# Kernel tuning notes

Measured on AMD Instinct MI355X. Metric: run time of the kernel, lower is better.

The kernel has to match this reference:

```python
import jax, jax.numpy as jnp
import numpy as np

B = 1024
NUM_FEATURES = 800  # 10*10 grid * 8 channels
L1, L2, L3, NUM_CLASSES = 1024, 15, 32, 1
STRIDE = 10  # max(1, (96+2*1-3)//(10-1))
VIS_THRESH = 0.0


def setup_inputs() -> dict:
    key = jax.random.key(0)
    ks = jax.random.split(key, 9)
    images = jax.random.normal(ks[0], (B, 3, 96, 96), dtype=jnp.float32)
    conv_w = jax.random.normal(ks[1], (8, 3, 3, 3), dtype=jnp.float32) * 0.1
    ft_w = jax.random.normal(ks[2], (NUM_FEATURES, L1), dtype=jnp.float32) * 0.1
    ft_b = jnp.zeros((L1,), dtype=jnp.float32)
    w1 = jax.random.normal(ks[3], (L2, L1), dtype=jnp.float32) * (1.0 / np.sqrt(L1))
    b1 = jax.random.normal(ks[4], (L2,), dtype=jnp.float32) * 0.01
    w2 = jax.random.normal(ks[5], (L3, L2), dtype=jnp.float32) * (1.0 / np.sqrt(L2))
    b2 = jax.random.normal(ks[6], (L3,), dtype=jnp.float32) * 0.01
    w3 = jax.random.normal(ks[7], (NUM_CLASSES, L3), dtype=jnp.float32) * (1.0 / np.sqrt(L3))
    b3 = jax.random.normal(ks[8], (NUM_CLASSES,), dtype=jnp.float32) * 0.01
    return {"images": images, "conv_w": conv_w, "ft_w": ft_w, "ft_b": ft_b,
            "w1": w1, "b1": b1, "w2": w2, "b2": b2, "w3": w3, "b3": b3}


def reference(images, conv_w, ft_w, ft_b, w1, b1, w2, b2, w3, b3):
    # Conv2d(3->8, k=3, stride=10, pad=1, no bias): [B,3,96,96] -> [B,8,10,10]
    x = jax.lax.conv_general_dilated(
        images, conv_w, window_strides=(STRIDE, STRIDE),
        padding=((1, 1), (1, 1)),
        dimension_numbers=("NCHW", "OIHW", "NCHW"))
    x = jnp.clip(x, -1.0, 1.0)  # Hardtanh
    # training-mode soft binarization
    binary = jax.nn.sigmoid(10.0 * (x - VIS_THRESH))
    bflat = binary.reshape(binary.shape[0], -1)  # [B, 800]
    # _to_sparse_features keeps only entries > 0.5; FeatureTransformer then does
    # a ragged gather-scale-sum == masked dense matmul with the FT weights.
    vals = jnp.where(bflat > 0.5, bflat, 0.0)
    features = vals @ ft_w + ft_b  # [B, L1]
    l0 = jnp.clip(features, 0.0, 1.0)
    h = L1 // 2
    s0, s1 = l0[:, :h], l0[:, h:]
    l0c = jnp.concatenate([s0 * s1, s0], axis=1) * (127.0 / 128.0)  # [B, L1]
    # SimpleClassifier: Linear->ReLU->Linear->ReLU->Linear
    h1 = jax.nn.relu(l0c @ w1.T + b1)
    h2 = jax.nn.relu(h1 @ w2.T + b2)
    out = h2 @ w3.T + b3  # [B, NUM_CLASSES]
    return out
```

## Files before the change

### kernel.cpp

```cpp
#include <hip/hip_runtime.h>

typedef unsigned short u16;
typedef unsigned int   u32;
typedef __attribute__((ext_vector_type(8))) short short8;
typedef __attribute__((ext_vector_type(4))) float f32x4;

__device__ __forceinline__ u16 f2bf(float f) {
    union { float f; u32 i; } v; v.f = f;
    u32 x = v.i;
    return (u16)((x + 0x7fffu + ((x >> 16) & 1u)) >> 16);
}
__device__ __forceinline__ float bf2f(u16 u) {
    union { u32 i; float f; } v; v.i = ((u32)u) << 16; return v.f;
}

__global__ __launch_bounds__(256) void k0_split(
    const float* __restrict__ ft_w,
    u16* __restrict__ bth, u16* __restrict__ btl)
{
    __shared__ float tile[32][33];
    int k0 = blockIdx.x * 32, n0 = blockIdx.y * 32;
    int tx = threadIdx.x & 31, ty = threadIdx.x >> 5;
    #pragma unroll
    for (int i = 0; i < 4; i++) {
        int k = ty + i * 8;
        tile[k][tx] = ft_w[(k0 + k) * 1024 + n0 + tx];
    }
    __syncthreads();
    #pragma unroll
    for (int i = 0; i < 4; i++) {
        int n = ty + i * 8;
        float wv = tile[tx][n];
        u16 hi = f2bf(wv);
        float lo = wv - bf2f(hi);
        bth[(n0 + n) * 800 + k0 + tx] = hi;
        btl[(n0 + n) * 800 + k0 + tx] = f2bf(lo);
    }
}

__global__ __launch_bounds__(256) void k1_conv(
    const float* __restrict__ images,
    const float* __restrict__ conv_w,
    u16* __restrict__ vh, u16* __restrict__ vl)
{
    __shared__ float img_s[3][29][96];
    __shared__ float w[216];

    int b = blockIdx.x;
    int t = threadIdx.x;
    if (t < 216) w[t] = conv_w[t];

    for (int i = t; i < 3 * 29 * 96; i += 256) {
        int ch  = i / (29 * 96);
        int rem = i - ch * (29 * 96);
        int lr  = rem / 96;
        int x   = rem - lr * 96;
        int ih  = 10 * ((lr + 1) / 3) + (lr + 1) % 3 - 1;
        img_s[ch][lr][x] = images[((b * 3 + ch) * 96 + ih) * 96 + x];
    }
    __syncthreads();

    for (int ridx = t; ridx < 800; ridx += 256) {
        int o  = ridx / 100;
        int p  = ridx - o * 100;
        int oh = p / 10;
        int ow = p - oh * 10;

        float sum = 0.0f;
        #pragma unroll
        for (int ic = 0; ic < 3; ic++) {
            const float* wc = &w[o * 27 + ic * 9];
            #pragma unroll
            for (int kh = 0; kh < 3; kh++) {
                int lr = 3 * oh + kh - 1;
                if (lr < 0) continue;
                #pragma unroll
                for (int kw = 0; kw < 3; kw++) {
                    int iw = ow * 10 + kw - 1;
                    if (iw < 0) continue;
                    sum = fmaf(img_s[ic][lr][iw], wc[kh * 3 + kw], sum);
                }
            }
        }
        float xc = fminf(fmaxf(sum, -1.0f), 1.0f);
        float binary = 1.0f / (1.0f + __expf(-10.0f * xc));
        float v = (binary > 0.5f) ? binary : 0.0f;
        u16 hi = f2bf(v);
        vh[b * 800 + ridx] = hi;
        vl[b * 800 + ridx] = f2bf(v - bf2f(hi));
    }
}

__global__ __launch_bounds__(256) void k2_mfma(
    const u16* __restrict__ Ah, const u16* __restrict__ Al,
    const u16* __restrict__ Bh, const u16* __restrict__ Bl,
    const float* __restrict__ bias,
    float* __restrict__ C)
{
    __shared__ u16 sAh[64 * 40], sAl[64 * 40], sBh[64 * 40], sBl[64 * 40];
    int t = threadIdx.x;
    int m0 = blockIdx.y * 64, n0 = blockIdx.x * 64;
    int w = t >> 6, lane = t & 63;
    int quad = lane >> 4, lo4 = lane & 15;
    int wm = (w >> 1) * 32, wn = (w & 1) * 32;

    int sr = t >> 2;
    int sq = t & 3;
    const u16* gAh = Ah + (m0 + sr) * 800 + sq * 8;
    const u16* gAl = Al + (m0 + sr) * 800 + sq * 8;
    const u16* gBh = Bh + (n0 + sr) * 800 + sq * 8;
    const u16* gBl = Bl + (n0 + sr) * 800 + sq * 8;
    int sdst = sr * 40 + sq * 8;

    f32x4 acc[2][2] = {};

    for (int k0 = 0; k0 < 800; k0 += 32) {
        *(uint4*)&sAh[sdst] = *(const uint4*)(gAh + k0);
        *(uint4*)&sAl[sdst] = *(const uint4*)(gAl + k0);
        *(uint4*)&sBh[sdst] = *(const uint4*)(gBh + k0);
        *(uint4*)&sBl[sdst] = *(const uint4*)(gBl + k0);
        __syncthreads();

        short8 a_h[2], a_l[2], b_h[2], b_l[2];
        #pragma unroll
        for (int f = 0; f < 2; f++) {
            int mi = (wm + f * 16 + lo4) * 40 + quad * 8;
            a_h[f] = *(const short8*)&sAh[mi];
            a_l[f] = *(const short8*)&sAl[mi];
            int ni = (wn + f * 16 + lo4) * 40 + quad * 8;
            b_h[f] = *(const short8*)&sBh[ni];
            b_l[f] = *(const short8*)&sBl[ni];
        }
        #pragma unroll
        for (int fm = 0; fm < 2; fm++)
            #pragma unroll
            for (int fn = 0; fn < 2; fn++) {
                acc[fm][fn] = __builtin_amdgcn_mfma_f32_16x16x32_bf16(a_h[fm], b_h[fn], acc[fm][fn], 0, 0, 0);
                acc[fm][fn] = __builtin_amdgcn_mfma_f32_16x16x32_bf16(a_h[fm], b_l[fn], acc[fm][fn], 0, 0, 0);
                acc[fm][fn] = __builtin_amdgcn_mfma_f32_16x16x32_bf16(a_l[fm], b_h[fn], acc[fm][fn], 0, 0, 0);
            }
        __syncthreads();
    }

    #pragma unroll
    for (int fm = 0; fm < 2; fm++) {
        #pragma unroll
        for (int fn = 0; fn < 2; fn++) {
            int n = n0 + wn + fn * 16 + lo4;
            float bv = bias[n];
            #pragma unroll
            for (int r = 0; r < 4; r++) {
                int m = m0 + wm + fm * 16 + quad * 4 + r;
                float v = acc[fm][fn][r] + bv;
                C[m * 1024 + n] = fminf(fmaxf(v, 0.f), 1.f);
            }
        }
    }
}

__global__ __launch_bounds__(256) void k3_tail(
    const float* __restrict__ l0,
    const float* __restrict__ w1,
    const float* __restrict__ b1,
    const float* __restrict__ w2,
    const float* __restrict__ b2,
    const float* __restrict__ w3,
    const float* __restrict__ b3,
    float* __restrict__ out)
{
    int wave = threadIdx.x >> 6;
    int lane = threadIdx.x & 63;
    int b = blockIdx.x * 4 + wave;
    const float* row = l0 + b * 1024;
    const float cc = 0.9921875f;

    float acc[15];
    #pragma unroll
    for (int j = 0; j < 15; j++) acc[j] = 0.f;

    for (int k = lane; k < 1024; k += 64) {
        float v;
        if (k < 512) v = row[k] * row[k + 512] * cc;
        else         v = row[k - 512] * cc;
        #pragma unroll
        for (int j = 0; j < 15; j++)
            acc[j] = fmaf(v, w1[j * 1024 + k], acc[j]);
    }

    #pragma unroll
    for (int j = 0; j < 15; j++) {
        #pragma unroll
        for (int m = 32; m >= 1; m >>= 1)
            acc[j] += __shfl_xor(acc[j], m, 64);
    }
    float h1[15];
    #pragma unroll
    for (int j = 0; j < 15; j++) h1[j] = fmaxf(acc[j] + b1[j], 0.f);

    float contrib = 0.f;
    if (lane < 32) {
        float h2 = b2[lane];
        #pragma unroll
        for (int j = 0; j < 15; j++) h2 = fmaf(h1[j], w2[lane * 15 + j], h2);
        h2 = fmaxf(h2, 0.f);
        contrib = h2 * w3[lane];
    }
    #pragma unroll
    for (int m = 32; m >= 1; m >>= 1) contrib += __shfl_xor(contrib, m, 64);

    if (lane == 0) out[b] = contrib + b3[0];
}

extern "C" void kernel_launch(void* const* d_in, const int* in_sizes, int n_in,
                              void* d_out, int out_size, void* d_ws, size_t ws_size,
                              hipStream_t stream) {
    const float* images = (const float*)d_in[0];
    const float* conv_w = (const float*)d_in[1];
    const float* ft_w   = (const float*)d_in[2];
    const float* ft_b   = (const float*)d_in[3];
    const float* w1     = (const float*)d_in[4];
    const float* b1     = (const float*)d_in[5];
    const float* w2     = (const float*)d_in[6];
    const float* b2     = (const float*)d_in[7];
    const float* w3     = (const float*)d_in[8];
    const float* b3     = (const float*)d_in[9];
    float* out = (float*)d_out;

    const int NV = 1024 * 800;
    u16* vh  = (u16*)d_ws;
    u16* vl  = vh + NV;
    u16* bth = vl + NV;
    u16* btl = bth + NV;
    float* l0 = (float*)(btl + NV);

    k0_split<<<dim3(25, 32), 256, 0, stream>>>(ft_w, bth, btl);
    k1_conv<<<1024, 256, 0, stream>>>(images, conv_w, vh, vl);
    k2_mfma<<<dim3(16, 16), 256, 0, stream>>>(vh, vl, bth, btl, ft_b, l0);
    k3_tail<<<256, 256, 0, stream>>>(l0, w1, b1, w2, b2, w3, b3, out);
}
```

Before: 215.0 us.

## Fuse weight split into conv kernel, halve GEMM N-tile, vectorize tail loads

```diff
diff --git a/kernel.cpp b/kernel.cpp
--- a/kernel.cpp
+++ b/kernel.cpp
@@ -14,40 +14,45 @@
     union { u32 i; float f; } v; v.i = ((u32)u) << 16; return v.f;
 }
 
-__global__ __launch_bounds__(256) void k0_split(
-    const float* __restrict__ ft_w,
-    u16* __restrict__ bth, u16* __restrict__ btl)
-{
-    __shared__ float tile[32][33];
-    int k0 = blockIdx.x * 32, n0 = blockIdx.y * 32;
-    int tx = threadIdx.x & 31, ty = threadIdx.x >> 5;
-    #pragma unroll
-    for (int i = 0; i < 4; i++) {
-        int k = ty + i * 8;
-        tile[k][tx] = ft_w[(k0 + k) * 1024 + n0 + tx];
-    }
-    __syncthreads();
-    #pragma unroll
-    for (int i = 0; i < 4; i++) {
-        int n = ty + i * 8;
-        float wv = tile[tx][n];
-        u16 hi = f2bf(wv);
-        float lo = wv - bf2f(hi);
-        bth[(n0 + n) * 800 + k0 + tx] = hi;
-        btl[(n0 + n) * 800 + k0 + tx] = f2bf(lo);
-    }
-}
-
-__global__ __launch_bounds__(256) void k1_conv(
+__global__ __launch_bounds__(256) void k1_conv_split(
     const float* __restrict__ images,
     const float* __restrict__ conv_w,
-    u16* __restrict__ vh, u16* __restrict__ vl)
+    const float* __restrict__ ft_w,
+    u16* __restrict__ vh, u16* __restrict__ vl,
+    u16* __restrict__ bth, u16* __restrict__ btl)
 {
     __shared__ float img_s[3][29][96];
     __shared__ float w[216];
+    __shared__ float tile[32][33];
+
+    int t = threadIdx.x;
+
+    if (blockIdx.x >= 1024) {
+        int n0 = (blockIdx.x - 1024) * 32;
+        int kk = t >> 5, nn = t & 31;
+        for (int k0 = 0; k0 < 800; k0 += 32) {
+            #pragma unroll
+            for (int i = 0; i < 4; i++) {
+                int k = kk + i * 8;
+                tile[k][nn] = ft_w[(k0 + k) * 1024 + n0 + nn];
+            }
+            __syncthreads();
+            int k = t & 31, n8 = t >> 5;
+            #pragma unroll
+            for (int i = 0; i < 4; i++) {
+                int n = n8 + i * 8;
+                float wv = tile[k][n];
+                u16 hi = f2bf(wv);
+                float lo = wv - bf2f(hi);
+                bth[(n0 + n) * 800 + k0 + k] = hi;
+                btl[(n0 + n) * 800 + k0 + k] = f2bf(lo);
+            }
+            __syncthreads();
+        }
+        return;
+    }
 
     int b = blockIdx.x;
-    int t = threadIdx.x;
     if (t < 216) w[t] = conv_w[t];
 
     for (int i = t; i < 3 * 29 * 96; i += 256) {
@@ -97,63 +102,62 @@
     const float* __restrict__ bias,
     float* __restrict__ C)
 {
-    __shared__ u16 sAh[64 * 40], sAl[64 * 40], sBh[64 * 40], sBl[64 * 40];
+    __shared__ u16 sAh[64 * 40], sAl[64 * 40];
+    __shared__ u16 sBh[32 * 40], sBl[32 * 40];
     int t = threadIdx.x;
-    int m0 = blockIdx.y * 64, n0 = blockIdx.x * 64;
+    int m0 = blockIdx.y * 64, n0 = blockIdx.x * 32;
     int w = t >> 6, lane = t & 63;
     int quad = lane >> 4, lo4 = lane & 15;
-    int wm = (w >> 1) * 32, wn = (w & 1) * 32;
-
-    int sr = t >> 2;
-    int sq = t & 3;
+    int wm = (w >> 1) * 32, wn = (w & 1) * 16;
+
+    int sr = t >> 2, sq = t & 3;
     const u16* gAh = Ah + (m0 + sr) * 800 + sq * 8;
     const u16* gAl = Al + (m0 + sr) * 800 + sq * 8;
-    const u16* gBh = Bh + (n0 + sr) * 800 + sq * 8;
-    const u16* gBl = Bl + (n0 + sr) * 800 + sq * 8;
-    int sdst = sr * 40 + sq * 8;
-
-    f32x4 acc[2][2] = {};
+    int adst = sr * 40 + sq * 8;
+    int barr = t >> 7;
+    int br = (t >> 2) & 31, bq = t & 3;
+    const u16* gB = (barr ? Bl : Bh) + (n0 + br) * 800 + bq * 8;
+    u16* sB = (barr ? sBl : sBh);
+    int bdst = br * 40 + bq * 8;
+
+    f32x4 acc[2] = {};
 
     for (int k0 = 0; k0 < 800; k0 += 32) {
-        *(uint4*)&sAh[sdst] = *(const uint4*)(gAh + k0);
-        *(uint4*)&sAl[sdst] = *(const uint4*)(gAl + k0);
-        *(uint4*)&sBh[sdst] = *(const uint4*)(gBh + k0);
-        *(uint4*)&sBl[sdst] = *(const uint4*)(gBl + k0);
+        *(uint4*)&sAh[adst] = *(const uint4*)(gAh + k0);
+        *(uint4*)&sAl[adst] = *(const uint4*)(gAl + k0);
+        *(uint4*)&sB[bdst]  = *(const uint4*)(gB + k0);
         __syncthreads();
 
-        short8 a_h[2], a_l[2], b_h[2], b_l[2];
+        short8 a_h[2], a_l[2], b_h, b_l;
         #pragma unroll
         for (int f = 0; f < 2; f++) {
             int mi = (wm + f * 16 + lo4) * 40 + quad * 8;
             a_h[f] = *(const short8*)&sAh[mi];
             a_l[f] = *(const short8*)&sAl[mi];
-            int ni = (wn + f * 16 + lo4) * 40 + quad * 8;
-            b_h[f] = *(const short8*)&sBh[ni];
-            b_l[f] = *(const short8*)&sBl[ni];
-        }
-        #pragma unroll
-        for (int fm = 0; fm < 2; fm++)
-            #pragma unroll
-            for (int fn = 0; fn < 2; fn++) {
-                acc[fm][fn] = __builtin_amdgcn_mfma_f32_16x16x32_bf16(a_h[fm], b_h[fn], acc[fm][fn], 0, 0, 0);
-                acc[fm][fn] = __builtin_amdgcn_mfma_f32_16x16x32_bf16(a_h[fm], b_l[fn], acc[fm][fn], 0, 0, 0);
-                acc[fm][fn] = __builtin_amdgcn_mfma_f32_16x16x32_bf16(a_l[fm], b_h[fn], acc[fm][fn], 0, 0, 0);
-            }
+        }
+        {
+            int ni = (wn + lo4) * 40 + quad * 8;
+            b_h = *(const short8*)&sBh[ni];
+            b_l = *(const short8*)&sBl[ni];
+        }
+        #pragma unroll
+        for (int fm = 0; fm < 2; fm++) {
+            acc[fm] = __builtin_amdgcn_mfma_f32_16x16x32_bf16(a_h[fm], b_h, acc[fm], 0, 0, 0);
+            acc[fm] = __builtin_amdgcn_mfma_f32_16x16x32_bf16(a_h[fm], b_l, acc[fm], 0, 0, 0);
+            acc[fm] = __builtin_amdgcn_mfma_f32_16x16x32_bf16(a_l[fm], b_h, acc[fm], 0, 0, 0);
+        }
         __syncthreads();
     }
 
+    int n = n0 + wn + lo4;
+    float bv = bias[n];
     #pragma unroll
     for (int fm = 0; fm < 2; fm++) {
         #pragma unroll
-        for (int fn = 0; fn < 2; fn++) {
-            int n = n0 + wn + fn * 16 + lo4;
-            float bv = bias[n];
-            #pragma unroll
-            for (int r = 0; r < 4; r++) {
-                int m = m0 + wm + fm * 16 + quad * 4 + r;
-                float v = acc[fm][fn][r] + bv;
-                C[m * 1024 + n] = fminf(fmaxf(v, 0.f), 1.f);
-            }
+        for (int r = 0; r < 4; r++) {
+            int m = m0 + wm + fm * 16 + quad * 4 + r;
+            float v = acc[fm][r] + bv;
+            C[m * 1024 + n] = fminf(fmaxf(v, 0.f), 1.f);
         }
     }
 }
@@ -178,13 +182,25 @@
     #pragma unroll
     for (int j = 0; j < 15; j++) acc[j] = 0.f;
 
-    for (int k = lane; k < 1024; k += 64) {
-        float v;
-        if (k < 512) v = row[k] * row[k + 512] * cc;
-        else         v = row[k - 512] * cc;
-        #pragma unroll
-        for (int j = 0; j < 15; j++)
-            acc[j] = fmaf(v, w1[j * 1024 + k], acc[j]);
+    #pragma unroll
+    for (int i = 0; i < 2; i++) {
+        int k4 = (lane + i * 64) * 4;
+        float4 x0 = *(const float4*)(row + k4);
+        float4 x1 = *(const float4*)(row + k4 + 512);
+        float4 va, vb;
+        va.x = x0.x * x1.x * cc; va.y = x0.y * x1.y * cc;
+        va.z = x0.z * x1.z * cc; va.w = x0.w * x1.w * cc;
+        vb.x = x0.x * cc; vb.y = x0.y * cc;
+        vb.z = x0.z * cc; vb.w = x0.w * cc;
+        #pragma unroll
+        for (int j = 0; j < 15; j++) {
+            float4 wa = *(const float4*)(w1 + j * 1024 + k4);
+            float4 wb = *(const float4*)(w1 + j * 1024 + k4 + 512);
+            acc[j] = fmaf(va.x, wa.x, acc[j]); acc[j] = fmaf(va.y, wa.y, acc[j]);
+            acc[j] = fmaf(va.z, wa.z, acc[j]); acc[j] = fmaf(va.w, wa.w, acc[j]);
+            acc[j] = fmaf(vb.x, wb.x, acc[j]); acc[j] = fmaf(vb.y, wb.y, acc[j]);
+            acc[j] = fmaf(vb.z, wb.z, acc[j]); acc[j] = fmaf(vb.w, wb.w, acc[j]);
+        }
     }
 
     #pragma unroll
@@ -233,8 +249,7 @@
     u16* btl = bth + NV;
     float* l0 = (float*)(btl + NV);
 
-    k0_split<<<dim3(25, 32), 256, 0, stream>>>(ft_w, bth, btl);
-    k1_conv<<<1024, 256, 0, stream>>>(images, conv_w, vh, vl);
-    k2_mfma<<<dim3(16, 16), 256, 0, stream>>>(vh, vl, bth, btl, ft_b, l0);
+    k1_conv_split<<<1056, 256, 0, stream>>>(images, conv_w, ft_w, vh, vl, bth, btl);
+    k2_mfma<<<dim3(32, 16), 256, 0, stream>>>(vh, vl, bth, btl, ft_b, l0);
     k3_tail<<<256, 256, 0, stream>>>(l0, w1, b1, w2, b2, w3, b3, out);
 }
```

Measured after the change: 229.5 us. 6.7% more time.
